# Performance work log

Hardware: AMD Instinct MI355X
Metric: run time of the kernel (lower is better)

Reference implementation:

```python
import jax, jax.numpy as jnp
import numpy as np

MARGIN = 0.1
SCALE_POS = 2.0
SCALE_NEG = 50.0
THRESH = 0.5
EPS = 1e-5


def setup_inputs() -> dict:
    key = jax.random.key(0)
    k1, k2 = jax.random.split(key)
    feats = jax.random.normal(k1, (4096, 2, 192), dtype=jnp.float32)
    labels = jax.random.randint(k2, (4096,), 0, 4096, dtype=jnp.int64)
    return {"feats": feats, "labels": labels}


def reference(feats, labels):
    B, n_utt, D = feats.shape
    lab = jnp.repeat(labels, n_utt)            # [N]
    f = feats.reshape(-1, D)                   # [N, D]
    N = f.shape[0]

    sim = f @ f.T                              # [N, N]
    # F.normalize(sim): L2-normalize each row, eps=1e-12
    row_norm = jnp.maximum(jnp.linalg.norm(sim, axis=1, keepdims=True), 1e-12)
    S = sim / row_norm

    same = lab[None, :] == lab[:, None]        # [N, N]
    pos_mask = same & (S < 1.0 - EPS)          # pos_pair_ (includes self if < 1-eps)
    neg_mask = ~same                           # neg_pair_

    min_pos = jnp.min(jnp.where(pos_mask, S, jnp.inf), axis=1)    # per-row min(pos_pair_)
    max_neg = jnp.max(jnp.where(neg_mask, S, -jnp.inf), axis=1)   # per-row max(neg_pair_)

    neg_keep = neg_mask & (S > (min_pos - MARGIN)[:, None])
    pos_keep = pos_mask & (S < (max_neg + MARGIN)[:, None])

    has_neg = jnp.any(neg_keep, axis=1)
    has_pos = jnp.any(pos_keep, axis=1)
    valid = has_neg & has_pos

    pos_sum = jnp.sum(jnp.where(pos_keep, jnp.exp(-SCALE_POS * (S - THRESH)), 0.0), axis=1)
    neg_sum = jnp.sum(jnp.where(neg_keep, jnp.exp(SCALE_NEG * (S - THRESH)), 0.0), axis=1)

    row_loss = (1.0 / SCALE_POS) * jnp.log1p(pos_sum) + (1.0 / SCALE_NEG) * jnp.log1p(neg_sum)
    loss = jnp.sum(jnp.where(valid, row_loss, 0.0)) / N

    # prec1 = percent of rows skipped for having no surviving negatives
    prec1 = jnp.sum(~has_neg).astype(jnp.float32) * 100.0 / N
    return loss, prec1
```

## Files before the change

### kernel.cpp

```cpp
#include <hip/hip_runtime.h>
#include <math.h>

typedef __bf16 bf16x8 __attribute__((ext_vector_type(8)));
typedef float  f32x4  __attribute__((ext_vector_type(4)));
typedef int    int4v  __attribute__((ext_vector_type(4)));

constexpr float MARGIN    = 0.1f;
constexpr float SCALE_POS = 2.0f;
constexpr float SCALE_NEG = 50.0f;
constexpr float THRESH    = 0.5f;
constexpr float ONE_EPS   = 1.0f - 1e-5f;
constexpr float LOG2E     = 1.4426950408889634f;
constexpr float BC        = -(SCALE_NEG * THRESH * LOG2E);
constexpr float VCUT_COEF = (36.0674f - 30.0f) / (SCALE_NEG * LOG2E);

constexpr int D      = 192;
constexpr int KS     = 6;
constexpr int RT     = 4;
constexpr int RPW    = 64;
constexpr int RPB    = 256;
constexpr int CSPLIT = 16;

constexpr int TILE_SH = KS * 64 * 8;

__device__ inline short f2bf(float x) {
  unsigned u = __float_as_uint(x);
  u += 0x7fffu + ((u >> 16) & 1u);
  return (short)(u >> 16);
}

__device__ inline float fast_exp2(float x) {
#if __has_builtin(__builtin_amdgcn_exp2f)
  return __builtin_amdgcn_exp2f(x);
#else
  return exp2f(x);
#endif
}

__device__ inline void async_copy16(const short* g, short* l) {
  __builtin_amdgcn_global_load_lds(
      (const __attribute__((address_space(1))) unsigned int*)(const void*)g,
      (__attribute__((address_space(3))) unsigned int*)(void*)l, 16, 0, 0);
}

__device__ inline void pin_frag(bf16x8& v) {
  int4v t = __builtin_bit_cast(int4v, v);
  asm volatile("" : "+v"(t));
  v = __builtin_bit_cast(bf16x8, t);
}

__global__ void k_pack(const float* __restrict__ f, short* __restrict__ pk, int total8) {
  int tid = blockIdx.x * blockDim.x + threadIdx.x;
  if (tid >= total8) return;
  int row = tid / 24;
  int j   = tid - row * 24;
  const float* src = f + (size_t)tid * 8;
  float4 a = *(const float4*)(src);
  float4 b = *(const float4*)(src + 4);
  union { short s[8]; int4v v; } o;
  o.s[0] = f2bf(a.x); o.s[1] = f2bf(a.y); o.s[2] = f2bf(a.z); o.s[3] = f2bf(a.w);
  o.s[4] = f2bf(b.x); o.s[5] = f2bf(b.y); o.s[6] = f2bf(b.z); o.s[7] = f2bf(b.w);
  int idx = (((row >> 4) * KS + (j >> 2)) * 64 + (j & 3) * 16 + (row & 15)) * 8;
  *(int4v*)(pk + idx) = o.v;
}

__global__ __launch_bounds__(1024) void k_buckets(
    const int* __restrict__ labs, int* __restrict__ hist_g, int* __restrict__ offs_g,
    int* __restrict__ bucket, float* __restrict__ accum, int n)
{
  __shared__ int histL[4096];
  __shared__ int offsL[4096];
  __shared__ int scanb[1024];
  const int t = threadIdx.x;

  if (t < 2) accum[t] = 0.f;
  for (int i = t; i < 4096; i += 1024) histL[i] = 0;
  __syncthreads();
  for (int i = t; i < n; i += 1024) atomicAdd(&histL[labs[i]], 1);
  __syncthreads();
  int base = t * 4;
  int v[4]; int ls = 0;
  for (int k = 0; k < 4; ++k) { v[k] = ls; ls += histL[base + k]; }
  scanb[t] = ls;
  __syncthreads();
  for (int o = 1; o < 1024; o <<= 1) {
    int x = (t >= o) ? scanb[t - o] : 0;
    __syncthreads();
    scanb[t] += x;
    __syncthreads();
  }
  int ebase = scanb[t] - ls;
  for (int k = 0; k < 4; ++k) {
    offsL[base + k] = ebase + v[k];
    offs_g[base + k] = ebase + v[k];
    hist_g[base + k] = histL[base + k];
  }
  __syncthreads();
  for (int i = t; i < 4096; i += 1024) histL[i] = 0;
  __syncthreads();
  for (int i = t; i < n; i += 1024) {
    int lab = labs[i];
    int p = atomicAdd(&histL[lab], 1);
    bucket[offsL[lab] + p] = i;
  }
}

__global__ __launch_bounds__(256, 2) void k_pass1(
    const short* __restrict__ pk, const int* __restrict__ labs,
    float* __restrict__ sumsqP, float* __restrict__ maxnegP,
    int N, int cps)
{
  __shared__ short ldsB[4][2][KS * 512];
  __shared__ int   ldsLab[512];

  const int tid  = threadIdx.x;
  const int lane = tid & 63;
  const int w    = tid >> 6;
  const int q    = lane >> 4;
  const int c    = lane & 15;
  const int cs   = blockIdx.x & (CSPLIT - 1);
  const int rbb  = blockIdx.x / CSPLIT;
  const int rowbase = rbb * RPB + w * RPW;
  const int col0 = cs * cps;
  const int ctile0 = col0 >> 4;
  const int ntiles = cps >> 4;

  for (int i = tid; i < cps; i += 256) ldsLab[i] = labs[(col0 + i) >> 1];

  {
    const short* g = pk + (size_t)ctile0 * TILE_SH + lane * 8;
#pragma unroll
    for (int k = 0; k < KS; ++k)
      async_copy16(g + k * 512, &ldsB[w][0][k * 512]);
  }

  bf16x8 afr[RT][KS];
#pragma unroll
  for (int rt = 0; rt < RT; ++rt)
#pragma unroll
    for (int ks = 0; ks < KS; ++ks) {
      afr[rt][ks] = *(const bf16x8*)(pk + (size_t)((rowbase >> 4) + rt) * TILE_SH + (ks * 64 + lane) * 8);
      pin_frag(afr[rt][ks]);
    }

  int labrow[RT][4];
#pragma unroll
  for (int rt = 0; rt < RT; ++rt)
#pragma unroll
    for (int rr = 0; rr < 4; ++rr)
      labrow[rt][rr] = labs[(rowbase + rt * 16 + q * 4 + rr) >> 1];

  float ssq[RT][4], mxn[RT][4];
#pragma unroll
  for (int rt = 0; rt < RT; ++rt)
#pragma unroll
    for (int rr = 0; rr < 4; ++rr) { ssq[rt][rr] = 0.f; mxn[rt][rr] = -INFINITY; }

  __syncthreads();

  for (int t = 0; t < ntiles; ++t) {
    asm volatile("s_waitcnt vmcnt(0)" ::: "memory");
    if (t + 1 < ntiles) {
      const short* g = pk + (size_t)(ctile0 + t + 1) * TILE_SH + lane * 8;
#pragma unroll
      for (int k = 0; k < KS; ++k)
        async_copy16(g + k * 512, &ldsB[w][(t + 1) & 1][k * 512]);
    }
    const int labcol = ldsLab[t * 16 + c];
    bf16x8 bfr[KS];
#pragma unroll
    for (int ks = 0; ks < KS; ++ks)
      bfr[ks] = *(const bf16x8*)&ldsB[w][t & 1][ks * 512 + lane * 8];
    f32x4 acc[RT];
#pragma unroll
    for (int rt = 0; rt < RT; ++rt) acc[rt] = 0.f;
#pragma unroll
    for (int ks = 0; ks < KS; ++ks)
#pragma unroll
      for (int rt = 0; rt < RT; ++rt)
        acc[rt] = __builtin_amdgcn_mfma_f32_16x16x32_bf16(afr[rt][ks], bfr[ks], acc[rt], 0, 0, 0);
#pragma unroll
    for (int rt = 0; rt < RT; ++rt)
#pragma unroll
      for (int rr = 0; rr < 4; ++rr) {
        float v = acc[rt][rr];
        ssq[rt][rr] = fmaf(v, v, ssq[rt][rr]);
        float vm = (labrow[rt][rr] == labcol) ? -INFINITY : v;
        mxn[rt][rr] = fmaxf(mxn[rt][rr], vm);
      }
  }

#pragma unroll
  for (int rt = 0; rt < RT; ++rt)
#pragma unroll
    for (int rr = 0; rr < 4; ++rr) {
      float s = ssq[rt][rr], m = mxn[rt][rr];
#pragma unroll
      for (int msk = 1; msk < 16; msk <<= 1) {
        s += __shfl_xor(s, msk, 64);
        m = fmaxf(m, __shfl_xor(m, msk, 64));
      }
      if (c == 0) {
        int row = rowbase + rt * 16 + q * 4 + rr;
        sumsqP[(size_t)cs * N + row] = s;
        maxnegP[(size_t)cs * N + row] = m;
      }
    }
}

__global__ void k_rowstats(
    const float* __restrict__ f, const int* __restrict__ labs,
    const float* __restrict__ sumsqP, const float* __restrict__ maxnegP,
    const int* __restrict__ offs, const int* __restrict__ hist, const int* __restrict__ bucket,
    float* __restrict__ nthr2, float* __restrict__ arow,
    float* __restrict__ validf, float* __restrict__ hasnegf, float* __restrict__ posloss,
    int N)
{
  const int lane = threadIdx.x & 63;
  const int row  = blockIdx.x * 4 + (threadIdx.x >> 6);

  float s = 0.f, m = -INFINITY;
  if (lane < CSPLIT) {
    s = sumsqP[(size_t)lane * N + row];
    m = maxnegP[(size_t)lane * N + row];
  }
#pragma unroll
  for (int msk = 1; msk < 64; msk <<= 1) {
    s += __shfl_xor(s, msk, 64);
    m = fmaxf(m, __shfl_xor(m, msk, 64));
  }
  float nrm = fmaxf(sqrtf(s), 1e-12f);
  float inv = 1.0f / nrm;
  float maxnegS = m * inv;
  float posth = fminf(ONE_EPS, maxnegS + MARGIN);

  const int lab = labs[row >> 1];
  const int beg = offs[lab], cnt = hist[lab];
  const float* fi = f + (size_t)row * D;
  float x0 = fi[lane], x1 = fi[lane + 64], x2 = fi[lane + 128];

  float minp = INFINITY, psum = 0.f; int pcnt = 0;
  for (int t = 0; t < cnt; ++t) {
    int smp = bucket[beg + t];
#pragma unroll
    for (int u = 0; u < 2; ++u) {
      const float* fj = f + (size_t)(smp * 2 + u) * D;
      float p = x0 * fj[lane] + x1 * fj[lane + 64] + x2 * fj[lane + 128];
#pragma unroll
      for (int msk = 1; msk < 64; msk <<= 1) p += __shfl_xor(p, msk, 64);
      minp = fminf(minp, p);
      float S = p * inv;
      if (S < posth) {
        psum += fast_exp2((THRESH - S) * (SCALE_POS * LOG2E));
        pcnt++;
      }
    }
  }

  float minS = minp * inv;
  float min_pos = (minS < ONE_EPS) ? minS : INFINITY;
  bool hneg = maxnegS > (min_pos - MARGIN);
  bool valid = hneg && (pcnt > 0);
  if (lane == 0) {
    nthr2[row]   = fmaxf((min_pos - MARGIN) * nrm, VCUT_COEF * nrm);
    arow[row]    = inv * (SCALE_NEG * LOG2E);
    validf[row]  = valid ? 1.f : 0.f;
    hasnegf[row] = hneg ? 1.f : 0.f;
    posloss[row] = valid ? ((1.0f / SCALE_POS) * log1pf(psum)) : 0.f;
  }
}

__global__ __launch_bounds__(256, 2) void k_pass2(
    const short* __restrict__ pk,
    const float* __restrict__ nthr2, const float* __restrict__ arow,
    const float* __restrict__ maxnegP,
    float* __restrict__ negsumP, int N, int cps)
{
  const int lane = threadIdx.x & 63;
  const int w    = threadIdx.x >> 6;
  const int q    = lane >> 4;
  const int c    = lane & 15;
  const int cs   = blockIdx.x & (CSPLIT - 1);
  const int rbb  = blockIdx.x / CSPLIT;
  const int rowbase = rbb * RPB + w * RPW;
  const int col0 = cs * cps;

  {
    int myrow = rowbase + lane;
    float mn = maxnegP[(size_t)cs * N + myrow];
    float th = nthr2[myrow];
    unsigned long long bal = __ballot(mn > th);
    if (bal == 0ull) {
      negsumP[(size_t)cs * N + myrow] = 0.f;
      return;
    }
  }

  bf16x8 afr[RT][KS];
#pragma unroll
  for (int rt = 0; rt < RT; ++rt)
#pragma unroll
    for (int ks = 0; ks < KS; ++ks)
      afr[rt][ks] = *(const bf16x8*)(pk + (size_t)((rowbase >> 4) + rt) * TILE_SH + (ks * 64 + lane) * 8);

  float nthrv[RT][4], arw[RT][4], ns[RT][4];
#pragma unroll
  for (int rt = 0; rt < RT; ++rt)
#pragma unroll
    for (int rr = 0; rr < 4; ++rr) {
      int row = rowbase + rt * 16 + q * 4 + rr;
      nthrv[rt][rr] = nthr2[row];
      arw[rt][rr]   = arow[row];
      ns[rt][rr]    = 0.f;
    }

  const short* bp = pk + (size_t)(col0 >> 4) * TILE_SH + lane * 8;
  for (int ct = 0; ct < cps; ct += 16, bp += TILE_SH) {
    bf16x8 bfr[KS];
#pragma unroll
    for (int ks = 0; ks < KS; ++ks) bfr[ks] = *(const bf16x8*)(bp + ks * 512);
    f32x4 acc[RT];
#pragma unroll
    for (int rt = 0; rt < RT; ++rt) acc[rt] = 0.f;
#pragma unroll
    for (int ks = 0; ks < KS; ++ks)
#pragma unroll
      for (int rt = 0; rt < RT; ++rt)
        acc[rt] = __builtin_amdgcn_mfma_f32_16x16x32_bf16(afr[rt][ks], bfr[ks], acc[rt], 0, 0, 0);
#pragma unroll
    for (int rt = 0; rt < RT; ++rt)
#pragma unroll
      for (int rr = 0; rr < 4; ++rr) {
        float v = acc[rt][rr];
        float e = fast_exp2(fmaf(v, arw[rt][rr], BC));
        ns[rt][rr] += (v > nthrv[rt][rr]) ? e : 0.f;
      }
  }

#pragma unroll
  for (int rt = 0; rt < RT; ++rt)
#pragma unroll
    for (int rr = 0; rr < 4; ++rr) {
      float sv = ns[rt][rr];
#pragma unroll
      for (int msk = 1; msk < 16; msk <<= 1) sv += __shfl_xor(sv, msk, 64);
      if (c == 0) {
        int row = rowbase + rt * 16 + q * 4 + rr;
        negsumP[(size_t)cs * N + row] = sv;
      }
    }
}

__global__ void k_final_part(const float* __restrict__ negsumP, const float* __restrict__ posloss,
                             const float* __restrict__ validf, const float* __restrict__ hasnegf,
                             float* __restrict__ accum, int N)
{
  int i = blockIdx.x * blockDim.x + threadIdx.x;
  float lacc = 0.f, nacc = 0.f;
  if (i < N) {
    float nsum = 0.f;
    for (int cs2 = 0; cs2 < CSPLIT; ++cs2) nsum += negsumP[(size_t)cs2 * N + i];
    lacc = validf[i] * (posloss[i] + (1.0f / SCALE_NEG) * log1pf(nsum));
    nacc = 1.0f - hasnegf[i];
  }
#pragma unroll
  for (int msk = 1; msk < 64; msk <<= 1) {
    lacc += __shfl_xor(lacc, msk, 64);
    nacc += __shfl_xor(nacc, msk, 64);
  }
  __shared__ float sl[4], sn[4];
  int wid = threadIdx.x >> 6, lane = threadIdx.x & 63;
  if (lane == 0) { sl[wid] = lacc; sn[wid] = nacc; }
  __syncthreads();
  if (threadIdx.x == 0) {
    float L = sl[0] + sl[1] + sl[2] + sl[3];
    float Nn = sn[0] + sn[1] + sn[2] + sn[3];
    atomicAdd(&accum[0], L);
    atomicAdd(&accum[1], Nn);
  }
}

__global__ void k_write(const float* __restrict__ accum, float* __restrict__ out, int N) {
  out[0] = accum[0] / (float)N;
  out[1] = accum[1] * 100.0f / (float)N;
}

extern "C" void kernel_launch(void* const* d_in, const int* in_sizes, int n_in,
                              void* d_out, int out_size, void* d_ws, size_t ws_size,
                              hipStream_t stream)
{
  (void)n_in; (void)out_size; (void)ws_size;
  const float* f    = (const float*)d_in[0];
  const int*   labs = (const int*)d_in[1];
  const int Bs = in_sizes[1];
  const int N  = 2 * Bs;

  char* ws = (char*)d_ws;
  size_t off = 0;
  auto alloc = [&](size_t bytes) -> void* {
    void* p = ws + off;
    off += (bytes + 255) & ~(size_t)255;
    return p;
  };
  short* pk      = (short*)alloc((size_t)N * D * sizeof(short));
  float* sumsqP  = (float*)alloc((size_t)CSPLIT * N * sizeof(float));
  float* maxnegP = (float*)alloc((size_t)CSPLIT * N * sizeof(float));
  float* negsumP = (float*)alloc((size_t)CSPLIT * N * sizeof(float));
  float* nthr2   = (float*)alloc((size_t)N * sizeof(float));
  float* arow    = (float*)alloc((size_t)N * sizeof(float));
  float* validf  = (float*)alloc((size_t)N * sizeof(float));
  float* hasnegf = (float*)alloc((size_t)N * sizeof(float));
  float* posloss = (float*)alloc((size_t)N * sizeof(float));
  int* hist   = (int*)alloc((size_t)Bs * sizeof(int));
  int* offs   = (int*)alloc((size_t)Bs * sizeof(int));
  int* bucket = (int*)alloc((size_t)Bs * sizeof(int));
  float* accum = (float*)alloc(2 * sizeof(float));

  const int total8 = N * 24;
  k_pack<<<(total8 + 255) / 256, 256, 0, stream>>>(f, pk, total8);
  k_buckets<<<1, 1024, 0, stream>>>(labs, hist, offs, bucket, accum, Bs);

  const int cps   = N / CSPLIT;
  const int grid1 = (N / RPB) * CSPLIT;
  k_pass1<<<grid1, 256, 0, stream>>>(pk, labs, sumsqP, maxnegP, N, cps);
  k_rowstats<<<N / 4, 256, 0, stream>>>(f, labs, sumsqP, maxnegP, offs, hist, bucket,
                                        nthr2, arow, validf, hasnegf, posloss, N);
  k_pass2<<<grid1, 256, 0, stream>>>(pk, nthr2, arow, maxnegP, negsumP, N, cps);
  k_final_part<<<(N + 255) / 256, 256, 0, stream>>>(negsumP, posloss, validf, hasnegf, accum, N);
  k_write<<<1, 1, 0, stream>>>(accum, (float*)d_out, N);
}
```

Baseline: 121.0 us.

## Replace LDS async staging with register double-buffered B tile loads

Pass1 no longer stages B tiles through LDS with global_load_lds and an explicit vmcnt wait. Both passes now prefetch B fragments directly into two register buffers, loading the next tile while the MFMAs for the current one run. Pass2 also pins its A fragments in registers. This removes LDS traffic and the per-tile wait barrier, but raises register pressure and assumes the tile count is even. The wrap-around prefetch of tile 0 is redundant but harmless.

```diff
diff --git a/kernel.cpp b/kernel.cpp
--- a/kernel.cpp
+++ b/kernel.cpp
@@ -35,12 +35,6 @@
 #else
   return exp2f(x);
 #endif
-}
-
-__device__ inline void async_copy16(const short* g, short* l) {
-  __builtin_amdgcn_global_load_lds(
-      (const __attribute__((address_space(1))) unsigned int*)(const void*)g,
-      (__attribute__((address_space(3))) unsigned int*)(void*)l, 16, 0, 0);
 }
 
 __device__ inline void pin_frag(bf16x8& v) {
@@ -110,8 +104,7 @@
     float* __restrict__ sumsqP, float* __restrict__ maxnegP,
     int N, int cps)
 {
-  __shared__ short ldsB[4][2][KS * 512];
-  __shared__ int   ldsLab[512];
+  __shared__ int ldsLab[512];
 
   const int tid  = threadIdx.x;
   const int lane = tid & 63;
@@ -127,13 +120,6 @@
 
   for (int i = tid; i < cps; i += 256) ldsLab[i] = labs[(col0 + i) >> 1];
 
-  {
-    const short* g = pk + (size_t)ctile0 * TILE_SH + lane * 8;
-#pragma unroll
-    for (int k = 0; k < KS; ++k)
-      async_copy16(g + k * 512, &ldsB[w][0][k * 512]);
-  }
-
   bf16x8 afr[RT][KS];
 #pragma unroll
   for (int rt = 0; rt < RT; ++rt)
@@ -158,27 +144,21 @@
 
   __syncthreads();
 
-  for (int t = 0; t < ntiles; ++t) {
-    asm volatile("s_waitcnt vmcnt(0)" ::: "memory");
-    if (t + 1 < ntiles) {
-      const short* g = pk + (size_t)(ctile0 + t + 1) * TILE_SH + lane * 8;
-#pragma unroll
-      for (int k = 0; k < KS; ++k)
-        async_copy16(g + k * 512, &ldsB[w][(t + 1) & 1][k * 512]);
-    }
+  auto loadB = [&](int tile, bf16x8 (&bf)[KS]) {
+    const short* bp = pk + (size_t)(ctile0 + tile) * TILE_SH + lane * 8;
+#pragma unroll
+    for (int ks = 0; ks < KS; ++ks) bf[ks] = *(const bf16x8*)(bp + ks * 512);
+  };
+  auto compute = [&](const bf16x8 (&bf)[KS], int t) {
     const int labcol = ldsLab[t * 16 + c];
-    bf16x8 bfr[KS];
+    f32x4 acc[RT];
+#pragma unroll
+    for (int rt = 0; rt < RT; ++rt) acc[rt] = 0.f;
 #pragma unroll
     for (int ks = 0; ks < KS; ++ks)
-      bfr[ks] = *(const bf16x8*)&ldsB[w][t & 1][ks * 512 + lane * 8];
-    f32x4 acc[RT];
-#pragma unroll
-    for (int rt = 0; rt < RT; ++rt) acc[rt] = 0.f;
-#pragma unroll
-    for (int ks = 0; ks < KS; ++ks)
 #pragma unroll
       for (int rt = 0; rt < RT; ++rt)
-        acc[rt] = __builtin_amdgcn_mfma_f32_16x16x32_bf16(afr[rt][ks], bfr[ks], acc[rt], 0, 0, 0);
+        acc[rt] = __builtin_amdgcn_mfma_f32_16x16x32_bf16(afr[rt][ks], bf[ks], acc[rt], 0, 0, 0);
 #pragma unroll
     for (int rt = 0; rt < RT; ++rt)
 #pragma unroll
@@ -188,6 +168,16 @@
         float vm = (labrow[rt][rr] == labcol) ? -INFINITY : v;
         mxn[rt][rr] = fmaxf(mxn[rt][rr], vm);
       }
+  };
+
+  bf16x8 b0[KS], b1[KS];
+  loadB(0, b0);
+  for (int t = 0; t < ntiles; t += 2) {
+    loadB(t + 1, b1);
+    compute(b0, t);
+    int nx = t + 2; nx = (nx < ntiles) ? nx : 0;
+    loadB(nx, b0);
+    compute(b1, t + 1);
   }
 
 #pragma unroll
@@ -283,7 +273,8 @@
   const int cs   = blockIdx.x & (CSPLIT - 1);
   const int rbb  = blockIdx.x / CSPLIT;
   const int rowbase = rbb * RPB + w * RPW;
-  const int col0 = cs * cps;
+  const int ctile0 = (cs * cps) >> 4;
+  const int ntiles = cps >> 4;
 
   {
     int myrow = rowbase + lane;
@@ -300,8 +291,10 @@
 #pragma unroll
   for (int rt = 0; rt < RT; ++rt)
 #pragma unroll
-    for (int ks = 0; ks < KS; ++ks)
+    for (int ks = 0; ks < KS; ++ks) {
       afr[rt][ks] = *(const bf16x8*)(pk + (size_t)((rowbase >> 4) + rt) * TILE_SH + (ks * 64 + lane) * 8);
+      pin_frag(afr[rt][ks]);
+    }
 
   float nthrv[RT][4], arw[RT][4], ns[RT][4];
 #pragma unroll
@@ -314,11 +307,12 @@
       ns[rt][rr]    = 0.f;
     }
 
-  const short* bp = pk + (size_t)(col0 >> 4) * TILE_SH + lane * 8;
-  for (int ct = 0; ct < cps; ct += 16, bp += TILE_SH) {
-    bf16x8 bfr[KS];
-#pragma unroll
-    for (int ks = 0; ks < KS; ++ks) bfr[ks] = *(const bf16x8*)(bp + ks * 512);
+  auto loadB = [&](int tile, bf16x8 (&bf)[KS]) {
+    const short* bp = pk + (size_t)(ctile0 + tile) * TILE_SH + lane * 8;
+#pragma unroll
+    for (int ks = 0; ks < KS; ++ks) bf[ks] = *(const bf16x8*)(bp + ks * 512);
+  };
+  auto compute = [&](const bf16x8 (&bf)[KS]) {
     f32x4 acc[RT];
 #pragma unroll
     for (int rt = 0; rt < RT; ++rt) acc[rt] = 0.f;
@@ -326,7 +320,7 @@
     for (int ks = 0; ks < KS; ++ks)
 #pragma unroll
       for (int rt = 0; rt < RT; ++rt)
-        acc[rt] = __builtin_amdgcn_mfma_f32_16x16x32_bf16(afr[rt][ks], bfr[ks], acc[rt], 0, 0, 0);
+        acc[rt] = __builtin_amdgcn_mfma_f32_16x16x32_bf16(afr[rt][ks], bf[ks], acc[rt], 0, 0, 0);
 #pragma unroll
     for (int rt = 0; rt < RT; ++rt)
 #pragma unroll
@@ -335,6 +329,16 @@
         float e = fast_exp2(fmaf(v, arw[rt][rr], BC));
         ns[rt][rr] += (v > nthrv[rt][rr]) ? e : 0.f;
       }
+  };
+
+  bf16x8 b0[KS], b1[KS];
+  loadB(0, b0);
+  for (int t = 0; t < ntiles; t += 2) {
+    loadB(t + 1, b1);
+    compute(b0);
+    int nx = t + 2; nx = (nx < ntiles) ? nx : 0;
+    loadB(nx, b0);
+    compute(b1);
   }
 
 #pragma unroll
```

Measured after the change: 111.0 us. 8.3% less time.
